# Performance work log

Hardware: AMD Instinct MI355X
Metric: run time of the kernel (lower is better)

Reference implementation:

```python
import jax, jax.numpy as jnp
import numpy as np

N = 50000      # nodes / stations
E = 600000     # edges
IN = 16        # in_channels
ED = 8         # edge_dim
HID = 128      # hidden
H = 4          # heads
C = HID // H   # 32 per-head channels
EMB = HID // 2 # station embedding dim
FEAT = HID - EMB
SLOPE = 0.2    # GATv2 LeakyReLU negative slope


def setup_inputs() -> dict:
    key = jax.random.key(0)
    ks = jax.random.split(key, 32)
    r = lambda i, shape, s=0.05: (jax.random.normal(ks[i], shape, jnp.float32) * s)
    inp = {
        "x": jax.random.normal(ks[0], (N, IN), jnp.float32),
        "node_idx": jax.random.randint(ks[1], (N,), 0, N),
        "edge_index": jax.random.randint(ks[2], (2, E), 0, N),
        "edge_attr": jax.random.normal(ks[3], (E, ED), jnp.float32),
        # params
        "emb": r(4, (N, EMB)),
        "W_in": r(5, (IN, FEAT)), "b_in": jnp.zeros((FEAT,), jnp.float32),
        # conv1 (GATv2: lin_l, lin_r, lin_edge, att, out bias)
        "Wl1": r(6, (HID, HID)), "bl1": jnp.zeros((HID,), jnp.float32),
        "Wr1": r(7, (HID, HID)), "br1": jnp.zeros((HID,), jnp.float32),
        "We1": r(8, (ED, HID)),  "be1": jnp.zeros((HID,), jnp.float32),
        "att1": r(9, (H, C)),    "bo1": jnp.zeros((HID,), jnp.float32),
        # conv2
        "Wl2": r(10, (HID, HID)), "bl2": jnp.zeros((HID,), jnp.float32),
        "Wr2": r(11, (HID, HID)), "br2": jnp.zeros((HID,), jnp.float32),
        "We2": r(12, (ED, HID)),  "be2": jnp.zeros((HID,), jnp.float32),
        "att2": r(13, (H, C)),    "bo2": jnp.zeros((HID,), jnp.float32),
        # layer norms
        "g1": jnp.ones((HID,), jnp.float32), "beta1": jnp.zeros((HID,), jnp.float32),
        "g2": jnp.ones((HID,), jnp.float32), "beta2": jnp.zeros((HID,), jnp.float32),
        # output head
        "W_out": r(14, (HID, 1)), "b_out": jnp.zeros((1,), jnp.float32),
    }
    return inp


def _gatv2(x, src, dst, ea, Wl, bl, Wr, br, We, be, att, bo):
    # x: [N,HID] -> per-head projections [N,H,C]
    xl = (x @ Wl + bl).reshape(-1, H, C)   # source transform
    xr = (x @ Wr + br).reshape(-1, H, C)   # target transform
    ee = (ea @ We + be).reshape(-1, H, C)  # edge transform [E,H,C]
    s = jax.nn.leaky_relu(xl[src] + xr[dst] + ee, SLOPE)  # [E,H,C]
    logit = jnp.einsum('ehc,hc->eh', s, att)              # [E,H]
    # segment softmax over destination node
    amax = jax.lax.stop_gradient(jax.ops.segment_max(logit, dst, num_segments=N))
    amax = jnp.where(jnp.isfinite(amax), amax, 0.0)
    ex = jnp.exp(logit - amax[dst])
    den = jax.ops.segment_sum(ex, dst, num_segments=N)
    alpha = ex / den[dst]                                  # [E,H]
    out = jax.ops.segment_sum(xl[src] * alpha[..., None], dst, num_segments=N)
    return out.reshape(-1, HID) + bo


def _ln(x, g, b):
    mu = x.mean(-1, keepdims=True)
    v = ((x - mu) ** 2).mean(-1, keepdims=True)
    return (x - mu) * jax.lax.rsqrt(v + 1e-5) * g + b


def reference(x, node_idx, edge_index, edge_attr, emb, W_in, b_in,
              Wl1, bl1, Wr1, br1, We1, be1, att1, bo1,
              Wl2, bl2, Wr2, br2, We2, be2, att2, bo2,
              g1, beta1, g2, beta2, W_out, b_out):
    src, dst = edge_index[0], edge_index[1]
    feat = jax.nn.relu(x @ W_in + b_in)                       # [N,FEAT]
    z = jnp.concatenate([feat, emb[node_idx]], axis=-1)       # [N,HID]
    h = jax.nn.relu(_gatv2(z, src, dst, edge_attr, Wl1, bl1, Wr1, br1, We1, be1, att1, bo1))
    z = _ln(z + h, g1, beta1)
    h = jax.nn.relu(_gatv2(z, src, dst, edge_attr, Wl2, bl2, Wr2, br2, We2, be2, att2, bo2))
    z = _ln(z + h, g2, beta2)
    return (z @ W_out + b_out).squeeze(-1)                    # [N]
```

## Files before the change

kernel.cpp:

```cpp
#include <hip/hip_runtime.h>
#include <hip/hip_bf16.h>

#define NN 50000
#define NE 600000
#define IND 16
#define EDD 8
#define HIDD 128
#define NH 4
#define CC 32
#define EMBD 64
#define FEATD 64
#define NB_SCAN ((NN + 255) / 256)

typedef __hip_bfloat16 bf16;
typedef __attribute__((ext_vector_type(8))) short bshort8;
typedef __attribute__((ext_vector_type(4))) float floatx4;
typedef __attribute__((ext_vector_type(2))) float f32x2;

__device__ __forceinline__ unsigned short f2bu(float f) {
    unsigned int u = __float_as_uint(f);
    u += 0x7fffu + ((u >> 16) & 1u);
    return (unsigned short)(u >> 16);
}

#if defined(__has_builtin)
#if __has_builtin(__builtin_amdgcn_fdot2_f32_bf16)
#define HAS_DOT2BF 1
#endif
#endif
#ifndef HAS_DOT2BF
#define HAS_DOT2BF 0
#endif

#if HAS_DOT2BF
typedef __attribute__((ext_vector_type(2))) __bf16 bfx2;
__device__ __forceinline__ float dot2bf(unsigned int a, unsigned int b, float c) {
    return __builtin_amdgcn_fdot2_f32_bf16(__builtin_bit_cast(bfx2, a),
                                           __builtin_bit_cast(bfx2, b), c, false);
}
#else
__device__ __forceinline__ float dot2bf(unsigned int a, unsigned int b, float c) {
    float a0 = __uint_as_float(a << 16), a1 = __uint_as_float(a & 0xffff0000u);
    float b0 = __uint_as_float(b << 16), b1 = __uint_as_float(b & 0xffff0000u);
    return __builtin_fmaf(a1, b1, __builtin_fmaf(a0, b0, c));
}
#endif

template <bool F32>
__device__ __forceinline__ float LD(const void* p, long long i) {
    if constexpr (F32) return ((const float*)p)[i];
    else return __bfloat162float(((const bf16*)p)[i]);
}

__device__ __forceinline__ bool is_f32(const int* cnt) { return *cnt > 8; }

__global__ void k_detinit(const unsigned short* __restrict__ x, int nhalf,
                          int* __restrict__ cnt, int* __restrict__ deg,
                          int* __restrict__ dcnt) {
    if (blockIdx.x == 0) {
        __shared__ int red[256];
        int hits = 0;
        for (int i = threadIdx.x; i < nhalf; i += 256)
            if ((x[i] & 0x7F80u) == 0x7F80u) hits++;
        red[threadIdx.x] = hits;
        __syncthreads();
        for (int o = 128; o; o >>= 1) {
            if (threadIdx.x < o) red[threadIdx.x] += red[threadIdx.x + o];
            __syncthreads();
        }
        if (threadIdx.x == 0) *cnt = red[0];
    } else {
        int gid = (blockIdx.x - 1) * 256 + threadIdx.x;
        if (gid < NN) deg[gid] = 0;
        if (blockIdx.x == 1 && threadIdx.x < 64) dcnt[threadIdx.x] = 0;
    }
}

__global__ void k_hist(const int* __restrict__ ei, int* __restrict__ deg, int* __restrict__ rank) {
    int e = blockIdx.x * blockDim.x + threadIdx.x;
    if (e < NE) rank[e] = atomicAdd(&deg[ei[NE + e]], 1);
}

__global__ void k_scan1(const int* __restrict__ deg, int* __restrict__ off,
                        int* __restrict__ bsum, int* __restrict__ dcnt,
                        int* __restrict__ rankd) {
    __shared__ int tile[256];
    __shared__ int lh[64];
    __shared__ int lbase[64];
    int t = threadIdx.x;
    int gid = blockIdx.x * 256 + t;
    if (t < 64) lh[t] = 0;
    __syncthreads();
    int v = (gid < NN) ? deg[gid] : 0;
    int b = 63 - min(v, 63);
    int lr = 0;
    if (gid < NN) lr = atomicAdd(&lh[b], 1);
    tile[t] = v;
    __syncthreads();
    if (t < 64) lbase[t] = lh[t] ? atomicAdd(&dcnt[t], lh[t]) : 0;
    #pragma unroll
    for (int o = 1; o < 256; o <<= 1) {
        int u = (t >= o) ? tile[t - o] : 0;
        __syncthreads();
        tile[t] += u;
        __syncthreads();
    }
    if (gid < NN) {
        off[gid] = tile[t] - v;
        rankd[gid] = lbase[b] + lr;
    }
    if (t == 255) bsum[blockIdx.x] = tile[255];
}
__global__ void k_scan2(int* __restrict__ bsum, int* __restrict__ dcnt,
                        int* __restrict__ dbase) {
    __shared__ int tile[256];
    __shared__ int d2[64];
    int t = threadIdx.x;
    int v = (t < NB_SCAN) ? bsum[t] : 0;
    tile[t] = v;
    int dv = (t < 64) ? dcnt[t] : 0;
    if (t < 64) d2[t] = dv;
    __syncthreads();
    #pragma unroll
    for (int o = 1; o < 256; o <<= 1) {
        int u = (t >= o) ? tile[t - o] : 0;
        __syncthreads();
        tile[t] += u;
        __syncthreads();
    }
    #pragma unroll
    for (int o = 1; o < 64; o <<= 1) {
        int u = (t >= o && t < 64) ? d2[t - o] : 0;
        __syncthreads();
        if (t < 64) d2[t] += u;
        __syncthreads();
    }
    if (t < NB_SCAN) bsum[t] = tile[t] - v;
    if (t < 64) dbase[t] = d2[t] - dv;
}
__global__ void k_scan3(int* __restrict__ off, const int* __restrict__ bsum,
                        const int* __restrict__ deg, const int* __restrict__ rankd,
                        const int* __restrict__ dbase, int* __restrict__ perm) {
    int gid = blockIdx.x * 256 + threadIdx.x;
    if (gid < NN) {
        off[gid] += bsum[blockIdx.x];
        int b = 63 - min(deg[gid], 63);
        perm[dbase[b] + rankd[gid]] = gid;
    }
    if (gid == 0) off[NN] = NE;
}

template <bool F32>
__device__ void fill_impl(const int* __restrict__ ei, const int* __restrict__ off,
                          const int* __restrict__ rank, int* __restrict__ esrc,
                          uint4* __restrict__ ea8, const void* ea) {
    int e = blockIdx.x * blockDim.x + threadIdx.x;
    if (e >= NE) return;
    if (e < 8) {
        esrc[NE + e] = 0;
        uint4 z; z.x = 0; z.y = 0; z.z = 0; z.w = 0;
        ea8[NE + e] = z;
    }
    int slot = off[ei[NE + e]] + rank[e];
    esrc[slot] = ei[e];
    uint4 v;
    if constexpr (F32) {
        const float4* ef = (const float4*)ea;
        float4 f0 = ef[2 * e], f1 = ef[2 * e + 1];
        v.x = (unsigned int)f2bu(f0.x) | ((unsigned int)f2bu(f0.y) << 16);
        v.y = (unsigned int)f2bu(f0.z) | ((unsigned int)f2bu(f0.w) << 16);
        v.z = (unsigned int)f2bu(f1.x) | ((unsigned int)f2bu(f1.y) << 16);
        v.w = (unsigned int)f2bu(f1.z) | ((unsigned int)f2bu(f1.w) << 16);
    } else {
        v = ((const uint4*)ea)[e];
    }
    ea8[slot] = v;
}
__global__ void k_fill(const int* cnt, const int* ei, const int* off, const int* rank,
                       int* esrc, uint4* ea8, const void* ea) {
    if (is_f32(cnt)) fill_impl<true>(ei, off, rank, esrc, ea8, ea);
    else             fill_impl<false>(ei, off, rank, esrc, ea8, ea);
}

template <bool F32>
__device__ void bzpw_impl(const void* x, const int* __restrict__ node_idx, const void* emb,
                          const void* W_in, const void* b_in, bf16* __restrict__ zb,
                          const void* Wl1, const void* bl1, const void* Wr1, const void* br1,
                          const void* Wl2, const void* bl2, const void* Wr2, const void* br2,
                          bf16* __restrict__ wbT, float* __restrict__ bias) {
    int t = threadIdx.x;
    if (blockIdx.x < NN) {
        int n = blockIdx.x;
        float val;
        if (t < FEATD) {
            float acc = LD<F32>(b_in, t);
            #pragma unroll
            for (int k = 0; k < IND; k++)
                acc += LD<F32>(x, (long long)n * IND + k) * LD<F32>(W_in, k * FEATD + t);
            val = fmaxf(acc, 0.f);
        } else {
            val = LD<F32>(emb, (long long)node_idx[n] * EMBD + (t - FEATD));
        }
        zb[n * HIDD + t] = __float2bfloat16(val);
    } else {
        int bid = blockIdx.x - NN;
        int layer = bid >> 8;
        int n = bid & 255;
        const void* W = layer ? (n < HIDD ? Wl2 : Wr2) : (n < HIDD ? Wl1 : Wr1);
        const void* b = layer ? (n < HIDD ? bl2 : br2) : (n < HIDD ? bl1 : br1);
        int nn = n & (HIDD - 1);
        wbT[(layer * 256 + n) * HIDD + t] = __float2bfloat16(LD<F32>(W, t * HIDD + nn));
        if (t == 0) bias[layer * 256 + n] = LD<F32>(b, nn);
    }
}
__global__ void k_bzpw(const int* cnt, const void* x, const int* node_idx, const void* emb,
                       const void* W_in, const void* b_in, bf16* zb,
                       const void* Wl1, const void* bl1, const void* Wr1, const void* br1,
                       const void* Wl2, const void* bl2, const void* Wr2, const void* br2,
                       bf16* wbT, float* bias) {
    if (is_f32(cnt)) bzpw_impl<true>(x, node_idx, emb, W_in, b_in, zb, Wl1, bl1, Wr1, br1,
                                     Wl2, bl2, Wr2, br2, wbT, bias);
    else             bzpw_impl<false>(x, node_idx, emb, W_in, b_in, zb, Wl1, bl1, Wr1, br1,
                                      Wl2, bl2, Wr2, br2, wbT, bias);
}

__global__ __launch_bounds__(256) void k_projmm(const bf16* __restrict__ zb,
                                                const bf16* __restrict__ wbT,
                                                const float* __restrict__ bias,
                                                bf16* __restrict__ xl, bf16* __restrict__ xr) {
    int wave = threadIdx.x >> 6, lane = threadIdx.x & 63;
    int m0 = blockIdx.x * 32;
    int n0 = wave * 64;
    int l15 = lane & 15, q = lane >> 4;
    bshort8 bfr[4][4];
    #pragma unroll
    for (int j = 0; j < 4; j++)
        #pragma unroll
        for (int s = 0; s < 4; s++)
            bfr[j][s] = *(const bshort8*)(wbT + ((n0 + j * 16 + l15) << 7) + s * 32 + q * 8);
    float bv[4];
    #pragma unroll
    for (int j = 0; j < 4; j++) bv[j] = bias[n0 + j * 16 + l15];
    const bf16* arow0 = zb + ((m0 + l15) << 7) + q * 8;
    const bf16* arow1 = arow0 + (16 << 7);
    bshort8 a0[4], a1[4];
    #pragma unroll
    for (int s = 0; s < 4; s++) a0[s] = *(const bshort8*)(arow0 + s * 32);
    #pragma unroll
    for (int s = 0; s < 4; s++) a1[s] = *(const bshort8*)(arow1 + s * 32);
    #pragma unroll
    for (int mi = 0; mi < 2; mi++) {
        floatx4 acc0 = {0.f, 0.f, 0.f, 0.f}, acc1 = acc0, acc2 = acc0, acc3 = acc0;
        #pragma unroll
        for (int s = 0; s < 4; s++) {
            bshort8 a = mi ? a1[s] : a0[s];
            acc0 = __builtin_amdgcn_mfma_f32_16x16x32_bf16(a, bfr[0][s], acc0, 0, 0, 0);
            acc1 = __builtin_amdgcn_mfma_f32_16x16x32_bf16(a, bfr[1][s], acc1, 0, 0, 0);
            acc2 = __builtin_amdgcn_mfma_f32_16x16x32_bf16(a, bfr[2][s], acc2, 0, 0, 0);
            acc3 = __builtin_amdgcn_mfma_f32_16x16x32_bf16(a, bfr[3][s], acc3, 0, 0, 0);
        }
        floatx4 accs[4] = {acc0, acc1, acc2, acc3};
        #pragma unroll
        for (int j = 0; j < 4; j++) {
            int colg = n0 + j * 16 + l15;
            bf16* dst = (colg < HIDD) ? (xl + colg) : (xr + (colg - HIDD));
            #pragma unroll
            for (int r = 0; r < 4; r++) {
                int rowc = m0 + mi * 16 + q * 4 + r;
                if (rowc < NN) dst[rowc << 7] = __float2bfloat16(accs[j][r] + bv[j]);
            }
        }
    }
}

__device__ __forceinline__ void edge_body(uint4 eu, uint2 xu, const unsigned int (*wp)[4],
                                          const float* base, const f32x2* at2,
                                          float mask, f32x2* acc, float& den) {
    f32x2 xv0, xv1;
    xv0.x = __uint_as_float(xu.x << 16); xv0.y = __uint_as_float(xu.x & 0xffff0000u);
    xv1.x = __uint_as_float(xu.y << 16); xv1.y = __uint_as_float(xu.y & 0xffff0000u);
    f32x2 e01, e23;
    {
        float c0 = base[0];
        c0 = dot2bf(eu.x, wp[0][0], c0);
        c0 = dot2bf(eu.y, wp[1][0], c0);
        c0 = dot2bf(eu.z, wp[2][0], c0);
        c0 = dot2bf(eu.w, wp[3][0], c0);
        float c1 = base[1];
        c1 = dot2bf(eu.x, wp[0][1], c1);
        c1 = dot2bf(eu.y, wp[1][1], c1);
        c1 = dot2bf(eu.z, wp[2][1], c1);
        c1 = dot2bf(eu.w, wp[3][1], c1);
        e01.x = c0; e01.y = c1;
        float c2 = base[2];
        c2 = dot2bf(eu.x, wp[0][2], c2);
        c2 = dot2bf(eu.y, wp[1][2], c2);
        c2 = dot2bf(eu.z, wp[2][2], c2);
        c2 = dot2bf(eu.w, wp[3][2], c2);
        float c3 = base[3];
        c3 = dot2bf(eu.x, wp[0][3], c3);
        c3 = dot2bf(eu.y, wp[1][3], c3);
        c3 = dot2bf(eu.z, wp[2][3], c3);
        c3 = dot2bf(eu.w, wp[3][3], c3);
        e23.x = c2; e23.y = c3;
    }
    f32x2 s0 = xv0 + e01;
    f32x2 s1 = xv1 + e23;
    s0 = __builtin_elementwise_max(s0, s0 * 0.2f);
    s1 = __builtin_elementwise_max(s1, s1 * 0.2f);
    f32x2 lsv = s0 * at2[0] + s1 * at2[1];
    float ls = lsv.x + lsv.y;
    ls += __shfl_xor(ls, 1);
    ls += __shfl_xor(ls, 2);
    ls += __shfl_xor(ls, 4);
    float ex = exp2f(ls) * mask;
    acc[0] += ex * xv0;
    acc[1] += ex * xv1;
    den += ex;
}

template <bool F32, bool LAST>
__device__ void gat_impl(const int* __restrict__ perm,
                         const int* __restrict__ off, const int* __restrict__ esrc,
                         const uint4* __restrict__ ea8,
                         const void* We, const void* be, const void* att,
                         const bf16* __restrict__ xl, const bf16* __restrict__ xr,
                         const void* bo, bf16* __restrict__ zb,
                         const void* g, const void* beta,
                         const void* Wo, const void* bout, void* out) {
    int wave = threadIdx.x >> 6;
    int half = (threadIdx.x >> 5) & 1;
    int lane5 = threadIdx.x & 31;
    int n = perm[blockIdx.x * 8 + wave * 2 + half];
    int c0 = lane5 << 2;
    unsigned int wp[4][4];
    #pragma unroll
    for (int p = 0; p < 4; p++)
        #pragma unroll
        for (int j = 0; j < 4; j++) {
            unsigned int lo = f2bu(LD<F32>(We, (2 * p) * HIDD + c0 + j));
            unsigned int hi = f2bu(LD<F32>(We, (2 * p + 1) * HIDD + c0 + j));
            wp[p][j] = lo | (hi << 16);
        }
    const float L2E = 1.4426950408889634f;
    f32x2 at2[2];
    at2[0].x = LD<F32>(att, c0 + 0) * L2E;
    at2[0].y = LD<F32>(att, c0 + 1) * L2E;
    at2[1].x = LD<F32>(att, c0 + 2) * L2E;
    at2[1].y = LD<F32>(att, c0 + 3) * L2E;
    uint2 xru = *(const uint2*)(xr + (n << 7) + c0);
    float xrv[4];
    xrv[0] = __uint_as_float(xru.x << 16);
    xrv[1] = __uint_as_float(xru.x & 0xffff0000u);
    xrv[2] = __uint_as_float(xru.y << 16);
    xrv[3] = __uint_as_float(xru.y & 0xffff0000u);
    float base[4];
    #pragma unroll
    for (int j = 0; j < 4; j++) base[j] = LD<F32>(be, c0 + j) + xrv[j];
    int lo = off[n], hi = off[n + 1];
    f32x2 accA[2] = {{0.f, 0.f}, {0.f, 0.f}}, accB[2] = {{0.f, 0.f}, {0.f, 0.f}};
    float denA = 0.f, denB = 0.f;
    if (lo < hi) {
        int sA = esrc[lo],      sB = esrc[lo + 1];
        uint4 eA = ea8[lo],     eB = ea8[lo + 1];
        int snA = esrc[lo + 2], snB = esrc[lo + 3];
        uint4 enA = ea8[lo + 2], enB = ea8[lo + 3];
        int s2A = esrc[lo + 4], s2B = esrc[lo + 5];
        uint4 e2A = ea8[lo + 4], e2B = ea8[lo + 5];
        uint2 xA = *(const uint2*)(xl + (sA << 7) + c0);
        uint2 xB = *(const uint2*)(xl + (sB << 7) + c0);
        uint2 xnA = *(const uint2*)(xl + (snA << 7) + c0);
        uint2 xnB = *(const uint2*)(xl + (snB << 7) + c0);
        for (int i = lo; i < hi; i += 2) {
            uint2 x2A = *(const uint2*)(xl + (s2A << 7) + c0);
            uint2 x2B = *(const uint2*)(xl + (s2B << 7) + c0);
            int s3A = esrc[i + 6],  s3B = esrc[i + 7];
            uint4 e3A = ea8[i + 6], e3B = ea8[i + 7];
            edge_body(eA, xA, wp, base, at2, 1.f, accA, denA);
            float mB = (i + 1 < hi) ? 1.f : 0.f;
            edge_body(eB, xB, wp, base, at2, mB, accB, denB);
            eA = enA; enA = e2A; e2A = e3A;
            eB = enB; enB = e2B; e2B = e3B;
            xA = xnA; xnA = x2A;
            xB = xnB; xnB = x2B;
            s2A = s3A; s2B = s3B;
        }
        accA[0] += accB[0];
        accA[1] += accB[1];
        denA += denB;
    }
    float inv = (denA > 0.f) ? 1.0f / denA : 0.f;
    uint2 zu = *(const uint2*)(zb + (n << 7) + c0);
    float zv[4];
    zv[0] = __uint_as_float(zu.x << 16);
    zv[1] = __uint_as_float(zu.x & 0xffff0000u);
    zv[2] = __uint_as_float(zu.y << 16);
    zv[3] = __uint_as_float(zu.y & 0xffff0000u);
    float accf[4] = {accA[0].x, accA[0].y, accA[1].x, accA[1].y};
    float v[4];
    float s = 0.f;
    #pragma unroll
    for (int j = 0; j < 4; j++) {
        float hv = fmaxf(accf[j] * inv + LD<F32>(bo, c0 + j), 0.f);
        v[j] = zv[j] + hv;
        s += v[j];
    }
    #pragma unroll
    for (int m = 16; m; m >>= 1) s += __shfl_xor(s, m);
    float mu = s * (1.f / HIDD);
    float s2 = 0.f;
    float dv[4];
    #pragma unroll
    for (int j = 0; j < 4; j++) { dv[j] = v[j] - mu; s2 += dv[j] * dv[j]; }
    #pragma unroll
    for (int m = 16; m; m >>= 1) s2 += __shfl_xor(s2, m);
    float rs = rsqrtf(s2 * (1.f / HIDD) + 1e-5f);
    float o[4];
    #pragma unroll
    for (int j = 0; j < 4; j++)
        o[j] = dv[j] * rs * LD<F32>(g, c0 + j) + LD<F32>(beta, c0 + j);
    if constexpr (!LAST) {
        uint2 pk;
        pk.x = (unsigned int)f2bu(o[0]) | ((unsigned int)f2bu(o[1]) << 16);
        pk.y = (unsigned int)f2bu(o[2]) | ((unsigned int)f2bu(o[3]) << 16);
        *(uint2*)(zb + (n << 7) + c0) = pk;
    } else {
        float po = 0.f;
        #pragma unroll
        for (int j = 0; j < 4; j++) po += o[j] * LD<F32>(Wo, c0 + j);
        #pragma unroll
        for (int m = 16; m; m >>= 1) po += __shfl_xor(po, m);
        if (lane5 == 0) {
            float r = po + LD<F32>(bout, 0);
            if constexpr (F32) ((float*)out)[n] = r;
            else               ((bf16*)out)[n] = __float2bfloat16(r);
        }
    }
}
__global__ void k_gat(const int* cnt, const int* perm, const int* off, const int* esrc,
                      const uint4* ea8, const void* We, const void* be, const void* att,
                      const bf16* xl, const bf16* xr, const void* bo, bf16* zb,
                      const void* g, const void* beta) {
    if (is_f32(cnt)) gat_impl<true, false>(perm, off, esrc, ea8, We, be, att, xl, xr, bo, zb, g, beta, nullptr, nullptr, nullptr);
    else             gat_impl<false, false>(perm, off, esrc, ea8, We, be, att, xl, xr, bo, zb, g, beta, nullptr, nullptr, nullptr);
}
__global__ void k_gat_last(const int* cnt, const int* perm, const int* off, const int* esrc,
                           const uint4* ea8, const void* We, const void* be, const void* att,
                           const bf16* xl, const bf16* xr, const void* bo, bf16* zb,
                           const void* g, const void* beta,
                           const void* Wo, const void* bout, void* out) {
    if (is_f32(cnt)) gat_impl<true, true>(perm, off, esrc, ea8, We, be, att, xl, xr, bo, zb, g, beta, Wo, bout, out);
    else             gat_impl<false, true>(perm, off, esrc, ea8, We, be, att, xl, xr, bo, zb, g, beta, Wo, bout, out);
}

extern "C" void kernel_launch(void* const* d_in, const int* in_sizes, int n_in,
                              void* d_out, int out_size, void* d_ws, size_t ws_size,
                              hipStream_t stream) {
    const void* x        = d_in[0];
    const int*  node_idx = (const int*)d_in[1];
    const int*  ei       = (const int*)d_in[2];
    const void* ea       = d_in[3];
    const void* emb      = d_in[4];
    const void* W_in     = d_in[5];
    const void* b_in     = d_in[6];
    const void* Wl1 = d_in[7];  const void* bl1 = d_in[8];
    const void* Wr1 = d_in[9];  const void* br1 = d_in[10];
    const void* We1 = d_in[11]; const void* be1 = d_in[12];
    const void* att1 = d_in[13]; const void* bo1 = d_in[14];
    const void* Wl2 = d_in[15]; const void* bl2 = d_in[16];
    const void* Wr2 = d_in[17]; const void* br2 = d_in[18];
    const void* We2 = d_in[19]; const void* be2 = d_in[20];
    const void* att2 = d_in[21]; const void* bo2 = d_in[22];
    const void* g1 = d_in[23]; const void* beta1 = d_in[24];
    const void* g2 = d_in[25]; const void* beta2 = d_in[26];
    const void* W_out = d_in[27]; const void* b_out = d_in[28];

    int*   cnt   = (int*)d_ws;
    uint4* ea8   = (uint4*)((char*)d_ws + 256);
    bf16*  zb    = (bf16*)(ea8 + NE + 8);
    bf16*  xl    = zb + NN * HIDD;
    bf16*  xr    = xl + NN * HIDD;
    bf16*  wbT   = xr + NN * HIDD;
    float* bias  = (float*)(wbT + 2 * 256 * HIDD);
    int*   off   = (int*)(bias + 512);
    int*   deg   = off + NN + 1;
    int*   rank  = deg + NN;
    int*   rankd = rank + NE;
    int*   perm  = rankd + NN;
    int*   esrc  = perm + NN;
    int*   bsum  = esrc + NE + 8;
    int*   dcnt  = bsum + 256;
    int*   dbase = dcnt + 64;

    int nhalf = in_sizes[0] < 16384 ? in_sizes[0] : 16384;
    k_detinit<<<NB_SCAN + 1, 256, 0, stream>>>((const unsigned short*)x, nhalf, cnt, deg, dcnt);
    k_hist<<<(NE + 255) / 256, 256, 0, stream>>>(ei, deg, rank);
    k_scan1<<<NB_SCAN, 256, 0, stream>>>(deg, off, bsum, dcnt, rankd);
    k_scan2<<<1, 256, 0, stream>>>(bsum, dcnt, dbase);
    k_scan3<<<NB_SCAN, 256, 0, stream>>>(off, bsum, deg, rankd, dbase, perm);
    k_bzpw<<<NN + 512, HIDD, 0, stream>>>(cnt, x, node_idx, emb, W_in, b_in, zb,
                                          Wl1, bl1, Wr1, br1, Wl2, bl2, Wr2, br2, wbT, bias);
    k_fill<<<(NE + 255) / 256, 256, 0, stream>>>(cnt, ei, off, rank, esrc, ea8, ea);

    k_projmm<<<(NN + 31) / 32, 256, 0, stream>>>(zb, wbT, bias, xl, xr);
    k_gat<<<NN / 8, 256, 0, stream>>>(cnt, perm, off, esrc, ea8, We1, be1, att1, xl, xr, bo1, zb, g1, beta1);

    k_projmm<<<(NN + 31) / 32, 256, 0, stream>>>(zb, wbT + 256 * HIDD, bias + 256, xl, xr);
    k_gat_last<<<NN / 8, 256, 0, stream>>>(cnt, perm, off, esrc, ea8, We2, be2, att2, xl, xr, bo2, zb,
                                           g2, beta2, W_out, b_out, d_out);
}
```

Measured before the change: 365.9 us.

## Fuse scan3, fill, embed and weight prep into one kernel; hoist GAT params

Merges scan finalisation, the edge CSR fill, the node embedding build and the weight transpose into a single multi-role launch, so several kernel launches and their gaps disappear. The fill computes offsets inline from the pre-scan values plus the block sums, so it no longer waits for a finalised offset array. Edge weights, attention (with the log2e factor folded in), biases and LN params are pre-packed once into small buffers, so the GAT kernels load vectors instead of converting per block. projmm now handles 64 rows per block and the embed path 8 nodes per 128-thread group. The extra code paths raise register pressure and make the prep kernel's blocks uneven in cost.

```diff
diff --git a/kernel.cpp b/kernel.cpp
--- a/kernel.cpp
+++ b/kernel.cpp
@@ -11,6 +11,10 @@
 #define EMBD 64
 #define FEATD 64
 #define NB_SCAN ((NN + 255) / 256)
+#define FILLB ((NE + 255) / 256)
+#define BZB (NN / 16)
+#define WPB 256
+#define PRMF 896
 
 typedef __hip_bfloat16 bf16;
 typedef __attribute__((ext_vector_type(8))) short bshort8;
@@ -81,7 +85,7 @@
     if (e < NE) rank[e] = atomicAdd(&deg[ei[NE + e]], 1);
 }
 
-__global__ void k_scan1(const int* __restrict__ deg, int* __restrict__ off,
+__global__ void k_scan1(const int* __restrict__ deg, int* __restrict__ off0,
                         int* __restrict__ bsum, int* __restrict__ dcnt,
                         int* __restrict__ rankd) {
     __shared__ int tile[256];
@@ -106,7 +110,7 @@
         __syncthreads();
     }
     if (gid < NN) {
-        off[gid] = tile[t] - v;
+        off0[gid] = tile[t] - v;
         rankd[gid] = lbase[b] + lr;
     }
     if (t == 255) bsum[blockIdx.x] = tile[255];
@@ -138,90 +142,148 @@
     if (t < NB_SCAN) bsum[t] = tile[t] - v;
     if (t < 64) dbase[t] = d2[t] - dv;
 }
-__global__ void k_scan3(int* __restrict__ off, const int* __restrict__ bsum,
-                        const int* __restrict__ deg, const int* __restrict__ rankd,
-                        const int* __restrict__ dbase, int* __restrict__ perm) {
-    int gid = blockIdx.x * 256 + threadIdx.x;
-    if (gid < NN) {
-        off[gid] += bsum[blockIdx.x];
-        int b = 63 - min(deg[gid], 63);
-        perm[dbase[b] + rankd[gid]] = gid;
-    }
-    if (gid == 0) off[NN] = NE;
-}
 
 template <bool F32>
-__device__ void fill_impl(const int* __restrict__ ei, const int* __restrict__ off,
-                          const int* __restrict__ rank, int* __restrict__ esrc,
-                          uint4* __restrict__ ea8, const void* ea) {
-    int e = blockIdx.x * blockDim.x + threadIdx.x;
-    if (e >= NE) return;
-    if (e < 8) {
-        esrc[NE + e] = 0;
-        uint4 z; z.x = 0; z.y = 0; z.z = 0; z.w = 0;
-        ea8[NE + e] = z;
-    }
-    int slot = off[ei[NE + e]] + rank[e];
-    esrc[slot] = ei[e];
-    uint4 v;
-    if constexpr (F32) {
-        const float4* ef = (const float4*)ea;
-        float4 f0 = ef[2 * e], f1 = ef[2 * e + 1];
-        v.x = (unsigned int)f2bu(f0.x) | ((unsigned int)f2bu(f0.y) << 16);
-        v.y = (unsigned int)f2bu(f0.z) | ((unsigned int)f2bu(f0.w) << 16);
-        v.z = (unsigned int)f2bu(f1.x) | ((unsigned int)f2bu(f1.y) << 16);
-        v.w = (unsigned int)f2bu(f1.z) | ((unsigned int)f2bu(f1.w) << 16);
-    } else {
-        v = ((const uint4*)ea)[e];
-    }
-    ea8[slot] = v;
-}
-__global__ void k_fill(const int* cnt, const int* ei, const int* off, const int* rank,
-                       int* esrc, uint4* ea8, const void* ea) {
-    if (is_f32(cnt)) fill_impl<true>(ei, off, rank, esrc, ea8, ea);
-    else             fill_impl<false>(ei, off, rank, esrc, ea8, ea);
-}
-
-template <bool F32>
-__device__ void bzpw_impl(const void* x, const int* __restrict__ node_idx, const void* emb,
+__device__ void prep_impl(const int* __restrict__ off0, const int* __restrict__ bsum,
+                          const int* __restrict__ deg, const int* __restrict__ rankd,
+                          const int* __restrict__ dbase, int* __restrict__ perm,
+                          int* __restrict__ offF,
+                          const int* __restrict__ ei, const int* __restrict__ rank,
+                          int* __restrict__ esrc, uint4* __restrict__ ea8, const void* ea,
+                          const void* x, const int* __restrict__ node_idx, const void* emb,
                           const void* W_in, const void* b_in, bf16* __restrict__ zb,
                           const void* Wl1, const void* bl1, const void* Wr1, const void* br1,
                           const void* Wl2, const void* bl2, const void* Wr2, const void* br2,
-                          bf16* __restrict__ wbT, float* __restrict__ bias) {
+                          bf16* __restrict__ wbT, float* __restrict__ bias,
+                          const void* We1, const void* att1, const void* be1, const void* bo1,
+                          const void* g1, const void* beta1,
+                          const void* We2, const void* att2, const void* be2, const void* bo2,
+                          const void* g2, const void* beta2,
+                          const void* Wo, const void* bout,
+                          unsigned int* __restrict__ wep, float* __restrict__ prm) {
+    int b = blockIdx.x;
     int t = threadIdx.x;
-    if (blockIdx.x < NN) {
-        int n = blockIdx.x;
-        float val;
-        if (t < FEATD) {
-            float acc = LD<F32>(b_in, t);
+    if (b < NB_SCAN) {
+        int gid = b * 256 + t;
+        if (gid < NN) {
+            offF[gid] = off0[gid] + bsum[b];
+            int bk = 63 - min(deg[gid], 63);
+            perm[dbase[bk] + rankd[gid]] = gid;
+        }
+        if (gid == 0) offF[NN] = NE;
+    } else if (b < NB_SCAN + FILLB) {
+        int e = (b - NB_SCAN) * 256 + t;
+        if (e >= NE) return;
+        if (e < 16) {
+            esrc[NE + e] = 0;
+            uint4 z; z.x = 0; z.y = 0; z.z = 0; z.w = 0;
+            ea8[NE + e] = z;
+        }
+        int dst = ei[NE + e];
+        int slot = off0[dst] + bsum[dst >> 8] + rank[e];
+        esrc[slot] = ei[e];
+        uint4 v;
+        if constexpr (F32) {
+            const float4* ef = (const float4*)ea;
+            float4 f0 = ef[2 * e], f1 = ef[2 * e + 1];
+            v.x = (unsigned int)f2bu(f0.x) | ((unsigned int)f2bu(f0.y) << 16);
+            v.y = (unsigned int)f2bu(f0.z) | ((unsigned int)f2bu(f0.w) << 16);
+            v.z = (unsigned int)f2bu(f1.x) | ((unsigned int)f2bu(f1.y) << 16);
+            v.w = (unsigned int)f2bu(f1.z) | ((unsigned int)f2bu(f1.w) << 16);
+        } else {
+            v = ((const uint4*)ea)[e];
+        }
+        ea8[slot] = v;
+    } else if (b < NB_SCAN + FILLB + BZB) {
+        int nb = (b - NB_SCAN - FILLB) * 16 + (t >> 7) * 8;
+        int t7 = t & 127;
+        if (t7 < FEATD) {
+            float w[IND];
             #pragma unroll
-            for (int k = 0; k < IND; k++)
-                acc += LD<F32>(x, (long long)n * IND + k) * LD<F32>(W_in, k * FEATD + t);
-            val = fmaxf(acc, 0.f);
+            for (int k = 0; k < IND; k++) w[k] = LD<F32>(W_in, k * FEATD + t7);
+            float bi = LD<F32>(b_in, t7);
+            #pragma unroll 2
+            for (int nd = 0; nd < 8; nd++) {
+                int n = nb + nd;
+                float acc = bi;
+                #pragma unroll
+                for (int k = 0; k < IND; k++)
+                    acc += LD<F32>(x, (long long)n * IND + k) * w[k];
+                zb[n * HIDD + t7] = __float2bfloat16(fmaxf(acc, 0.f));
+            }
         } else {
-            val = LD<F32>(emb, (long long)node_idx[n] * EMBD + (t - FEATD));
-        }
-        zb[n * HIDD + t] = __float2bfloat16(val);
+            #pragma unroll 2
+            for (int nd = 0; nd < 8; nd++) {
+                int n = nb + nd;
+                zb[n * HIDD + t7] = __float2bfloat16(
+                    LD<F32>(emb, (long long)node_idx[n] * EMBD + (t7 - FEATD)));
+            }
+        }
+    } else if (b < NB_SCAN + FILLB + BZB + WPB) {
+        int bid2 = (b - NB_SCAN - FILLB - BZB) * 2 + (t >> 7);
+        int layer = bid2 >> 8;
+        int n2 = bid2 & 255;
+        int t7 = t & 127;
+        const void* W = layer ? (n2 < HIDD ? Wl2 : Wr2) : (n2 < HIDD ? Wl1 : Wr1);
+        const void* bb = layer ? (n2 < HIDD ? bl2 : br2) : (n2 < HIDD ? bl1 : br1);
+        int nn = n2 & (HIDD - 1);
+        wbT[(layer * 256 + n2) * HIDD + t7] = __float2bfloat16(LD<F32>(W, t7 * HIDD + nn));
+        if (t7 == 0) bias[layer * 256 + n2] = LD<F32>(bb, nn);
     } else {
-        int bid = blockIdx.x - NN;
-        int layer = bid >> 8;
-        int n = bid & 255;
-        const void* W = layer ? (n < HIDD ? Wl2 : Wr2) : (n < HIDD ? Wl1 : Wr1);
-        const void* b = layer ? (n < HIDD ? bl2 : br2) : (n < HIDD ? bl1 : br1);
-        int nn = n & (HIDD - 1);
-        wbT[(layer * 256 + n) * HIDD + t] = __float2bfloat16(LD<F32>(W, t * HIDD + nn));
-        if (t == 0) bias[layer * 256 + n] = LD<F32>(b, nn);
-    }
-}
-__global__ void k_bzpw(const int* cnt, const void* x, const int* node_idx, const void* emb,
+        int layer = b - (NB_SCAN + FILLB + BZB + WPB);
+        const void* We = layer ? We2 : We1;
+        const void* att = layer ? att2 : att1;
+        const void* be = layer ? be2 : be1;
+        const void* bo = layer ? bo2 : bo1;
+        const void* g  = layer ? g2 : g1;
+        const void* bt = layer ? beta2 : beta1;
+        if (t < 128) {
+            int lane5 = t >> 2, j = t & 3, c0 = lane5 * 4;
+            #pragma unroll
+            for (int p = 0; p < 4; p++) {
+                unsigned int lo_ = f2bu(LD<F32>(We, (2 * p) * HIDD + c0 + j));
+                unsigned int hi_ = f2bu(LD<F32>(We, (2 * p + 1) * HIDD + c0 + j));
+                wep[layer * 512 + lane5 * 16 + p * 4 + j] = lo_ | (hi_ << 16);
+            }
+        } else {
+            int t2 = t - 128;
+            float* Pp = prm + layer * PRMF;
+            Pp[t2]        = LD<F32>(att, t2) * 1.4426950408889634f;
+            Pp[128 + t2]  = LD<F32>(be, t2);
+            Pp[256 + t2]  = LD<F32>(bo, t2);
+            Pp[384 + t2]  = LD<F32>(g, t2);
+            Pp[512 + t2]  = LD<F32>(bt, t2);
+            if (layer) {
+                Pp[640 + t2] = LD<F32>(Wo, t2);
+                if (t2 == 0) Pp[768] = LD<F32>(bout, 0);
+            }
+        }
+    }
+}
+__global__ void k_prep(const int* cnt, const int* off0, const int* bsum, const int* deg,
+                       const int* rankd, const int* dbase, int* perm, int* offF,
+                       const int* ei, const int* rank, int* esrc, uint4* ea8, const void* ea,
+                       const void* x, const int* node_idx, const void* emb,
                        const void* W_in, const void* b_in, bf16* zb,
                        const void* Wl1, const void* bl1, const void* Wr1, const void* br1,
                        const void* Wl2, const void* bl2, const void* Wr2, const void* br2,
-                       bf16* wbT, float* bias) {
-    if (is_f32(cnt)) bzpw_impl<true>(x, node_idx, emb, W_in, b_in, zb, Wl1, bl1, Wr1, br1,
-                                     Wl2, bl2, Wr2, br2, wbT, bias);
-    else             bzpw_impl<false>(x, node_idx, emb, W_in, b_in, zb, Wl1, bl1, Wr1, br1,
-                                      Wl2, bl2, Wr2, br2, wbT, bias);
+                       bf16* wbT, float* bias,
+                       const void* We1, const void* att1, const void* be1, const void* bo1,
+                       const void* g1, const void* beta1,
+                       const void* We2, const void* att2, const void* be2, const void* bo2,
+                       const void* g2, const void* beta2,
+                       const void* Wo, const void* bout,
+                       unsigned int* wep, float* prm) {
+    if (is_f32(cnt))
+        prep_impl<true>(off0, bsum, deg, rankd, dbase, perm, offF, ei, rank, esrc, ea8, ea,
+                        x, node_idx, emb, W_in, b_in, zb, Wl1, bl1, Wr1, br1,
+                        Wl2, bl2, Wr2, br2, wbT, bias, We1, att1, be1, bo1, g1, beta1,
+                        We2, att2, be2, bo2, g2, beta2, Wo, bout, wep, prm);
+    else
+        prep_impl<false>(off0, bsum, deg, rankd, dbase, perm, offF, ei, rank, esrc, ea8, ea,
+                         x, node_idx, emb, W_in, b_in, zb, Wl1, bl1, Wr1, br1,
+                         Wl2, bl2, Wr2, br2, wbT, bias, We1, att1, be1, bo1, g1, beta1,
+                         We2, att2, be2, bo2, g2, beta2, Wo, bout, wep, prm);
 }
 
 __global__ __launch_bounds__(256) void k_projmm(const bf16* __restrict__ zb,
@@ -229,7 +291,6 @@
                                                 const float* __restrict__ bias,
                                                 bf16* __restrict__ xl, bf16* __restrict__ xr) {
     int wave = threadIdx.x >> 6, lane = threadIdx.x & 63;
-    int m0 = blockIdx.x * 32;
     int n0 = wave * 64;
     int l15 = lane & 15, q = lane >> 4;
     bshort8 bfr[4][4];
@@ -241,33 +302,37 @@
     float bv[4];
     #pragma unroll
     for (int j = 0; j < 4; j++) bv[j] = bias[n0 + j * 16 + l15];
-    const bf16* arow0 = zb + ((m0 + l15) << 7) + q * 8;
-    const bf16* arow1 = arow0 + (16 << 7);
-    bshort8 a0[4], a1[4];
-    #pragma unroll
-    for (int s = 0; s < 4; s++) a0[s] = *(const bshort8*)(arow0 + s * 32);
-    #pragma unroll
-    for (int s = 0; s < 4; s++) a1[s] = *(const bshort8*)(arow1 + s * 32);
-    #pragma unroll
-    for (int mi = 0; mi < 2; mi++) {
-        floatx4 acc0 = {0.f, 0.f, 0.f, 0.f}, acc1 = acc0, acc2 = acc0, acc3 = acc0;
+    #pragma unroll
+    for (int mt = 0; mt < 2; mt++) {
+        int m0 = blockIdx.x * 64 + mt * 32;
+        const bf16* arow0 = zb + ((m0 + l15) << 7) + q * 8;
+        const bf16* arow1 = arow0 + (16 << 7);
+        bshort8 a0[4], a1[4];
         #pragma unroll
-        for (int s = 0; s < 4; s++) {
-            bshort8 a = mi ? a1[s] : a0[s];
-            acc0 = __builtin_amdgcn_mfma_f32_16x16x32_bf16(a, bfr[0][s], acc0, 0, 0, 0);
-            acc1 = __builtin_amdgcn_mfma_f32_16x16x32_bf16(a, bfr[1][s], acc1, 0, 0, 0);
-            acc2 = __builtin_amdgcn_mfma_f32_16x16x32_bf16(a, bfr[2][s], acc2, 0, 0, 0);
-            acc3 = __builtin_amdgcn_mfma_f32_16x16x32_bf16(a, bfr[3][s], acc3, 0, 0, 0);
-        }
-        floatx4 accs[4] = {acc0, acc1, acc2, acc3};
+        for (int s = 0; s < 4; s++) a0[s] = *(const bshort8*)(arow0 + s * 32);
         #pragma unroll
-        for (int j = 0; j < 4; j++) {
-            int colg = n0 + j * 16 + l15;
-            bf16* dst = (colg < HIDD) ? (xl + colg) : (xr + (colg - HIDD));
+        for (int s = 0; s < 4; s++) a1[s] = *(const bshort8*)(arow1 + s * 32);
+        #pragma unroll
+        for (int mi = 0; mi < 2; mi++) {
+            floatx4 acc0 = {0.f, 0.f, 0.f, 0.f}, acc1 = acc0, acc2 = acc0, acc3 = acc0;
             #pragma unroll
-            for (int r = 0; r < 4; r++) {
-                int rowc = m0 + mi * 16 + q * 4 + r;
-                if (rowc < NN) dst[rowc << 7] = __float2bfloat16(accs[j][r] + bv[j]);
+            for (int s = 0; s < 4; s++) {
+                bshort8 a = mi ? a1[s] : a0[s];
+                acc0 = __builtin_amdgcn_mfma_f32_16x16x32_bf16(a, bfr[0][s], acc0, 0, 0, 0);
+                acc1 = __builtin_amdgcn_mfma_f32_16x16x32_bf16(a, bfr[1][s], acc1, 0, 0, 0);
+                acc2 = __builtin_amdgcn_mfma_f32_16x16x32_bf16(a, bfr[2][s], acc2, 0, 0, 0);
+                acc3 = __builtin_amdgcn_mfma_f32_16x16x32_bf16(a, bfr[3][s], acc3, 0, 0, 0);
+            }
+            floatx4 accs[4] = {acc0, acc1, acc2, acc3};
+            #pragma unroll
+            for (int j = 0; j < 4; j++) {
+                int colg = n0 + j * 16 + l15;
+                bf16* dst = (colg < HIDD) ? (xl + colg) : (xr + (colg - HIDD));
+                #pragma unroll
+                for (int r = 0; r < 4; r++) {
+                    int rowc = m0 + mi * 16 + q * 4 + r;
+                    if (rowc < NN) dst[rowc << 7] = __float2bfloat16(accs[j][r] + bv[j]);
+                }
             }
         }
     }
@@ -319,44 +384,39 @@
     den += ex;
 }
 
-template <bool F32, bool LAST>
-__device__ void gat_impl(const int* __restrict__ perm,
+template <bool LAST>
+__device__ __forceinline__ void gat_impl(const int* __restrict__ perm,
                          const int* __restrict__ off, const int* __restrict__ esrc,
                          const uint4* __restrict__ ea8,
-                         const void* We, const void* be, const void* att,
+                         const unsigned int* __restrict__ wep,
+                         const float* __restrict__ P,
                          const bf16* __restrict__ xl, const bf16* __restrict__ xr,
-                         const void* bo, bf16* __restrict__ zb,
-                         const void* g, const void* beta,
-                         const void* Wo, const void* bout, void* out) {
+                         bf16* __restrict__ zb, void* out, bool f32out) {
     int wave = threadIdx.x >> 6;
     int half = (threadIdx.x >> 5) & 1;
     int lane5 = threadIdx.x & 31;
     int n = perm[blockIdx.x * 8 + wave * 2 + half];
     int c0 = lane5 << 2;
     unsigned int wp[4][4];
-    #pragma unroll
-    for (int p = 0; p < 4; p++)
-        #pragma unroll
-        for (int j = 0; j < 4; j++) {
-            unsigned int lo = f2bu(LD<F32>(We, (2 * p) * HIDD + c0 + j));
-            unsigned int hi = f2bu(LD<F32>(We, (2 * p + 1) * HIDD + c0 + j));
-            wp[p][j] = lo | (hi << 16);
-        }
-    const float L2E = 1.4426950408889634f;
+    {
+        const uint4* w4 = (const uint4*)(wep + lane5 * 16);
+        uint4 wa = w4[0], wb = w4[1], wc = w4[2], wd = w4[3];
+        wp[0][0] = wa.x; wp[0][1] = wa.y; wp[0][2] = wa.z; wp[0][3] = wa.w;
+        wp[1][0] = wb.x; wp[1][1] = wb.y; wp[1][2] = wb.z; wp[1][3] = wb.w;
+        wp[2][0] = wc.x; wp[2][1] = wc.y; wp[2][2] = wc.z; wp[2][3] = wc.w;
+        wp[3][0] = wd.x; wp[3][1] = wd.y; wp[3][2] = wd.z; wp[3][3] = wd.w;
+    }
+    float4 atv = *(const float4*)(P + c0);
     f32x2 at2[2];
-    at2[0].x = LD<F32>(att, c0 + 0) * L2E;
-    at2[0].y = LD<F32>(att, c0 + 1) * L2E;
-    at2[1].x = LD<F32>(att, c0 + 2) * L2E;
-    at2[1].y = LD<F32>(att, c0 + 3) * L2E;
+    at2[0].x = atv.x; at2[0].y = atv.y;
+    at2[1].x = atv.z; at2[1].y = atv.w;
+    float4 bev = *(const float4*)(P + 128 + c0);
     uint2 xru = *(const uint2*)(xr + (n << 7) + c0);
-    float xrv[4];
-    xrv[0] = __uint_as_float(xru.x << 16);
-    xrv[1] = __uint_as_float(xru.x & 0xffff0000u);
-    xrv[2] = __uint_as_float(xru.y << 16);
-    xrv[3] = __uint_as_float(xru.y & 0xffff0000u);
     float base[4];
-    #pragma unroll
-    for (int j = 0; j < 4; j++) base[j] = LD<F32>(be, c0 + j) + xrv[j];
+    base[0] = bev.x + __uint_as_float(xru.x << 16);
+    base[1] = bev.y + __uint_as_float(xru.x & 0xffff0000u);
+    base[2] = bev.z + __uint_as_float(xru.y << 16);
+    base[3] = bev.w + __uint_as_float(xru.y & 0xffff0000u);
     int lo = off[n], hi = off[n + 1];
     f32x2 accA[2] = {{0.f, 0.f}, {0.f, 0.f}}, accB[2] = {{0.f, 0.f}, {0.f, 0.f}};
     float denA = 0.f, denB = 0.f;
@@ -397,60 +457,63 @@
     zv[2] = __uint_as_float(zu.y << 16);
     zv[3] = __uint_as_float(zu.y & 0xffff0000u);
     float accf[4] = {accA[0].x, accA[0].y, accA[1].x, accA[1].y};
+    float4 bo4 = *(const float4*)(P + 256 + c0);
+    float bov[4] = {bo4.x, bo4.y, bo4.z, bo4.w};
     float v[4];
     float s = 0.f;
     #pragma unroll
     for (int j = 0; j < 4; j++) {
-        float hv = fmaxf(accf[j] * inv + LD<F32>(bo, c0 + j), 0.f);
+        float hv = fmaxf(accf[j] * inv + bov[j], 0.f);
         v[j] = zv[j] + hv;
         s += v[j];
     }
     #pragma unroll
     for (int m = 16; m; m >>= 1) s += __shfl_xor(s, m);
     float mu = s * (1.f / HIDD);
-    float s2 = 0.f;
+    float s2v = 0.f;
     float dv[4];
     #pragma unroll
-    for (int j = 0; j < 4; j++) { dv[j] = v[j] - mu; s2 += dv[j] * dv[j]; }
-    #pragma unroll
-    for (int m = 16; m; m >>= 1) s2 += __shfl_xor(s2, m);
-    float rs = rsqrtf(s2 * (1.f / HIDD) + 1e-5f);
+    for (int j = 0; j < 4; j++) { dv[j] = v[j] - mu; s2v += dv[j] * dv[j]; }
+    #pragma unroll
+    for (int m = 16; m; m >>= 1) s2v += __shfl_xor(s2v, m);
+    float rs = rsqrtf(s2v * (1.f / HIDD) + 1e-5f);
+    float4 g4 = *(const float4*)(P + 384 + c0);
+    float4 bt4 = *(const float4*)(P + 512 + c0);
+    float gv[4] = {g4.x, g4.y, g4.z, g4.w};
+    float btv[4] = {bt4.x, bt4.y, bt4.z, bt4.w};
     float o[4];
     #pragma unroll
     for (int j = 0; j < 4; j++)
-        o[j] = dv[j] * rs * LD<F32>(g, c0 + j) + LD<F32>(beta, c0 + j);
+        o[j] = dv[j] * rs * gv[j] + btv[j];
     if constexpr (!LAST) {
         uint2 pk;
         pk.x = (unsigned int)f2bu(o[0]) | ((unsigned int)f2bu(o[1]) << 16);
         pk.y = (unsigned int)f2bu(o[2]) | ((unsigned int)f2bu(o[3]) << 16);
         *(uint2*)(zb + (n << 7) + c0) = pk;
     } else {
+        float4 wo4 = *(const float4*)(P + 640 + c0);
+        float wov[4] = {wo4.x, wo4.y, wo4.z, wo4.w};
         float po = 0.f;
         #pragma unroll
-        for (int j = 0; j < 4; j++) po += o[j] * LD<F32>(Wo, c0 + j);
+        for (int j = 0; j < 4; j++) po += o[j] * wov[j];
         #pragma unroll
         for (int m = 16; m; m >>= 1) po += __shfl_xor(po, m);
         if (lane5 == 0) {
-            float r = po + LD<F32>(bout, 0);
-            if constexpr (F32) ((float*)out)[n] = r;
-            else               ((bf16*)out)[n] = __float2bfloat16(r);
-        }
-    }
-}
-__global__ void k_gat(const int* cnt, const int* perm, const int* off, const int* esrc,
-                      const uint4* ea8, const void* We, const void* be, const void* att,
-                      const bf16* xl, const bf16* xr, const void* bo, bf16* zb,
-                      const void* g, const void* beta) {
-    if (is_f32(cnt)) gat_impl<true, false>(perm, off, esrc, ea8, We, be, att, xl, xr, bo, zb, g, beta, nullptr, nullptr, nullptr);
-    else             gat_impl<false, false>(perm, off, esrc, ea8, We, be, att, xl, xr, bo, zb, g, beta, nullptr, nullptr, nullptr);
+            float r = po + P[768];
+            if (f32out) ((float*)out)[n] = r;
+            else        ((bf16*)out)[n] = __float2bfloat16(r);
+        }
+    }
+}
+__global__ void k_gat(const int* perm, const int* off, const int* esrc,
+                      const uint4* ea8, const unsigned int* wep, const float* prm,
+                      const bf16* xl, const bf16* xr, bf16* zb) {
+    gat_impl<false>(perm, off, esrc, ea8, wep, prm, xl, xr, zb, nullptr, false);
 }
 __global__ void k_gat_last(const int* cnt, const int* perm, const int* off, const int* esrc,
-                           const uint4* ea8, const void* We, const void* be, const void* att,
-                           const bf16* xl, const bf16* xr, const void* bo, bf16* zb,
-                           const void* g, const void* beta,
-                           const void* Wo, const void* bout, void* out) {
-    if (is_f32(cnt)) gat_impl<true, true>(perm, off, esrc, ea8, We, be, att, xl, xr, bo, zb, g, beta, Wo, bout, out);
-    else             gat_impl<false, true>(perm, off, esrc, ea8, We, be, att, xl, xr, bo, zb, g, beta, Wo, bout, out);
+                           const uint4* ea8, const unsigned int* wep, const float* prm,
+                           const bf16* xl, const bf16* xr, bf16* zb, void* out) {
+    gat_impl<true>(perm, off, esrc, ea8, wep, prm, xl, xr, zb, out, is_f32(cnt));
 }
 
 extern "C" void kernel_launch(void* const* d_in, const int* in_sizes, int n_in,
@@ -477,35 +540,41 @@
 
     int*   cnt   = (int*)d_ws;
     uint4* ea8   = (uint4*)((char*)d_ws + 256);
-    bf16*  zb    = (bf16*)(ea8 + NE + 8);
+    bf16*  zb    = (bf16*)(ea8 + NE + 16);
     bf16*  xl    = zb + NN * HIDD;
     bf16*  xr    = xl + NN * HIDD;
     bf16*  wbT   = xr + NN * HIDD;
     float* bias  = (float*)(wbT + 2 * 256 * HIDD);
-    int*   off   = (int*)(bias + 512);
-    int*   deg   = off + NN + 1;
+    unsigned int* wep = (unsigned int*)(bias + 512);
+    float* prm   = (float*)(wep + 1024);
+    int*   off0  = (int*)(prm + 2 * PRMF);
+    int*   offF  = off0 + NN + 1;
+    int*   deg   = offF + NN + 1;
     int*   rank  = deg + NN;
     int*   rankd = rank + NE;
     int*   perm  = rankd + NN;
     int*   esrc  = perm + NN;
-    int*   bsum  = esrc + NE + 8;
+    int*   bsum  = esrc + NE + 16;
     int*   dcnt  = bsum + 256;
     int*   dbase = dcnt + 64;
 
     int nhalf = in_sizes[0] < 16384 ? in_sizes[0] : 16384;
     k_detinit<<<NB_SCAN + 1, 256, 0, stream>>>((const unsigned short*)x, nhalf, cnt, deg, dcnt);
-    k_hist<<<(NE + 255) / 256, 256, 0, stream>>>(ei, deg, rank);
-    k_scan1<<<NB_SCAN, 256, 0, stream>>>(deg, off, bsum, dcnt, rankd);
+    k_hist<<<FILLB, 256, 0, stream>>>(ei, deg, rank);
+    k_scan1<<<NB_SCAN, 256, 0, stream>>>(deg, off0, bsum, dcnt, rankd);
     k_scan2<<<1, 256, 0, stream>>>(bsum, dcnt, dbase);
-    k_scan3<<<NB_SCAN, 256, 0, stream>>>(off, bsum, deg, rankd, dbase, perm);
-    k_bzpw<<<NN + 512, HIDD, 0, stream>>>(cnt, x, node_idx, emb, W_in, b_in, zb,
-                                          Wl1, bl1, Wr1, br1, Wl2, bl2, Wr2, br2, wbT, bias);
-    k_fill<<<(NE + 255) / 256, 256, 0, stream>>>(cnt, ei, off, rank, esrc, ea8, ea);
-
-    k_projmm<<<(NN + 31) / 32, 256, 0, stream>>>(zb, wbT, bias, xl, xr);
-    k_gat<<<NN / 8, 256, 0, stream>>>(cnt, perm, off, esrc, ea8, We1, be1, att1, xl, xr, bo1, zb, g1, beta1);
-
-    k_projmm<<<(NN + 31) / 32, 256, 0, stream>>>(zb, wbT + 256 * HIDD, bias + 256, xl, xr);
-    k_gat_last<<<NN / 8, 256, 0, stream>>>(cnt, perm, off, esrc, ea8, We2, be2, att2, xl, xr, bo2, zb,
-                                           g2, beta2, W_out, b_out, d_out);
-}
+    k_prep<<<NB_SCAN + FILLB + BZB + WPB + 2, 256, 0, stream>>>(
+        cnt, off0, bsum, deg, rankd, dbase, perm, offF, ei, rank, esrc, ea8, ea,
+        x, node_idx, emb, W_in, b_in, zb,
+        Wl1, bl1, Wr1, br1, Wl2, bl2, Wr2, br2, wbT, bias,
+        We1, att1, be1, bo1, g1, beta1,
+        We2, att2, be2, bo2, g2, beta2,
+        W_out, b_out, wep, prm);
+
+    k_projmm<<<(NN + 63) / 64, 256, 0, stream>>>(zb, wbT, bias, xl, xr);
+    k_gat<<<NN / 8, 256, 0, stream>>>(perm, offF, esrc, ea8, wep, prm, xl, xr, zb);
+
+    k_projmm<<<(NN + 63) / 64, 256, 0, stream>>>(zb, wbT + 256 * HIDD, bias + 256, xl, xr);
+    k_gat_last<<<NN / 8, 256, 0, stream>>>(cnt, perm, offF, esrc, ea8, wep + 512, prm + PRMF,
+                                           xl, xr, zb, d_out);
+}
```

New measurement: 359.9 us. No clear change (-1.6%).
